# Performance work log

Hardware: AMD Instinct MI355X
Metric: run time of the kernel (lower is better)

Reference implementation:

```python
import jax, jax.numpy as jnp
import numpy as np

N, K, D_LOCAL, P, BINS = 8192, 32, 256, 128, 64
N_RBF, REL_CLIP = 16, 32
REL_DIM = 2 * REL_CLIP + 2  # 65 rel-pos buckets + 1 'different chain/batch' bucket
N_ATOMS = 5


def _normalize(v, eps=1e-8):
    return v / (jnp.linalg.norm(v, axis=-1, keepdims=True) + eps)


def _frames(pos):
    # Gram-Schmidt backbone frames from N, CA, C atoms. pos: [N, A, 3]
    n, ca, c = pos[:, 0], pos[:, 1], pos[:, 2]
    e1 = _normalize(c - ca)
    v2 = n - ca
    e2 = _normalize(v2 - jnp.sum(v2 * e1, -1, keepdims=True) * e1)
    e3 = jnp.cross(e1, e2)
    return jnp.stack([e1, e2, e3], axis=-1)  # [N, 3, 3], columns are basis


def setup_inputs() -> dict:
    key = jax.random.key(0)
    ks = jax.random.split(key, 16)
    inp = {
        "local": jax.random.normal(ks[0], (N, D_LOCAL), jnp.float32),
        "pos": jax.random.normal(ks[1], (N, N_ATOMS, 3), jnp.float32) * 3.0,
        "neighbours": jax.random.randint(ks[2], (N, K), 0, N, jnp.int32),
        "resi": jnp.arange(N, dtype=jnp.int32),
        "chain": jnp.zeros((N,), jnp.int32),
        "batch": jnp.zeros((N,), jnp.int32),
        "mask": jnp.ones((N,), bool),
    }
    def lin(k, fan_in, fan_out):
        return jax.random.normal(k, (fan_in, fan_out), jnp.float32) / np.sqrt(fan_in)
    inp["W_relpos"] = lin(ks[3], REL_DIM, P)
    inp["W_dist"] = lin(ks[4], N_RBF, P)
    inp["W_dir"] = lin(ks[5], 3, P)
    inp["W_rot"] = lin(ks[6], 9, P)
    inp["W_pvec"] = lin(ks[7], N_ATOMS * 3, P)
    inp["W_loc_i"] = lin(ks[8], D_LOCAL, P)
    inp["W_loc_j"] = lin(ks[9], D_LOCAL, P)
    inp["ln_scale"] = jnp.ones((P,), jnp.float32)
    inp["ln_bias"] = jnp.zeros((P,), jnp.float32)
    inp["W1"] = lin(ks[10], P, 2 * P)
    inp["b1"] = jnp.zeros((2 * P,), jnp.float32)
    inp["W2"] = lin(ks[11], 2 * P, BINS) * 0.02  # final layer (small init; zeros in original)
    inp["b2"] = jnp.zeros((BINS,), jnp.float32)
    return inp


def reference(local, pos, neighbours, resi, chain, batch, mask,
              W_relpos, W_dist, W_dir, W_rot, W_pvec, W_loc_i, W_loc_j,
              ln_scale, ln_bias, W1, b1, W2, b2):
    idx = jnp.where(neighbours < 0, 0, neighbours)          # safe gather index [N, K]
    m = mask.astype(jnp.float32)
    pair_mask = m[:, None] * m[idx] * (neighbours != -1)    # [N, K]

    # --- sequence relative position (one-hot, clipped to +/-32) ---
    rel = jnp.clip(resi[idx] - resi[:, None], -REL_CLIP, REL_CLIP) + REL_CLIP
    same = (chain[:, None] == chain[idx]) & (batch[:, None] == batch[idx])
    code = jnp.where(same, rel, REL_DIM - 1)
    f_rel = jax.nn.one_hot(code, REL_DIM, dtype=jnp.float32)  # [N, K, 66]

    # --- geometric features ---
    ca = pos[:, 1]                                           # [N, 3]
    R = _frames(pos)                                         # [N, 3, 3]
    dvec = ca[idx] - ca[:, None]                             # [N, K, 3]
    d = jnp.linalg.norm(dvec, axis=-1)                       # [N, K]
    centers = jnp.linspace(0.0, 22.0, N_RBF)
    sigma = 22.0 / N_RBF
    f_dist = jnp.exp(-((d[..., None] - centers) ** 2) / (2 * sigma ** 2))  # [N,K,16]
    unit = dvec / (d[..., None] + 1e-8)
    f_dir = jnp.einsum("nab,nka->nkb", R, unit)              # [N, K, 3] direction in local frame
    f_rot = jnp.einsum("nab,nkac->nkbc", R, R[idx]).reshape(d.shape + (9,))  # R_i^T R_j
    pv = pos[idx] - ca[:, None, None]                        # [N, K, A, 3]
    f_pv = jnp.einsum("nab,nkma->nkmb", R, pv).reshape(d.shape + (N_ATOMS * 3,))

    # --- multi-branch linear fusion ---
    pair = (f_rel @ W_relpos + f_dist @ W_dist + f_dir @ W_dir
            + f_rot @ W_rot + f_pv @ W_pvec
            + (local @ W_loc_i)[:, None] + (local @ W_loc_j)[idx])
    pair = pair * pair_mask[..., None]

    # --- LayerNorm (create_scale/offset, eps=1e-5) ---
    mu = jnp.mean(pair, axis=-1, keepdims=True)
    var = jnp.mean((pair - mu) ** 2, axis=-1, keepdims=True)
    pair = (pair - mu) * jax.lax.rsqrt(var + 1e-5) * ln_scale + ln_bias

    # --- MLP + log_softmax ---
    hidden = jax.nn.gelu(pair @ W1 + b1)
    distogram = hidden @ W2 + b2                             # [N, K, 64]
    return jax.nn.log_softmax(distogram, axis=-1)
```

## Files before the change

### kernel.cpp

```cpp
#include <hip/hip_runtime.h>
#include <hip/hip_bf16.h>
#include <math.h>

#define N_NODES 8192
#define KNBR    32
#define PDIM    128
#define BINS    64
#define REL_CLIP 32
#define REL_DIM  66
#define RSTR    136

typedef unsigned short ushort_t;
typedef short v8s  __attribute__((ext_vector_type(8)));
typedef float v4f  __attribute__((ext_vector_type(4)));

__device__ __forceinline__ ushort_t f2bf(float f) {
    union { __hip_bfloat16 b; ushort_t u; } cv;
    cv.b = __float2bfloat16(f);
    return cv.u;
}
__device__ __forceinline__ unsigned int pk2bf(float lo, float hiv) {
    union { __hip_bfloat162 h2; unsigned int u; } cv;
    cv.h2 = __float22bfloat162_rn(make_float2(lo, hiv));
    return cv.u;
}
__device__ __forceinline__ float gelu_sig(float x) {
    float e = exp2f(-2.4554045f * x);
    return x / (1.f + e);
}

__global__ __launch_bounds__(256) void prep_kernel(
    const float* __restrict__ W_dist, const float* __restrict__ W_dir,
    const float* __restrict__ W_rot, const float* __restrict__ W_pvec,
    const float* __restrict__ W_relpos,
    const float* __restrict__ W1, const float* __restrict__ W2,
    const float* __restrict__ W_loc_i, const float* __restrict__ W_loc_j,
    const float* __restrict__ ln_scale, const float* __restrict__ ln_bias,
    const float* __restrict__ b1,
    ushort_t* __restrict__ Wcomb, ushort_t* __restrict__ W1Ts,
    ushort_t* __restrict__ W2T, ushort_t* __restrict__ W_locT,
    float* __restrict__ b1p)
{
    int idx = blockIdx.x * 256 + threadIdx.x;
    if (idx < 16384) {
        int col = idx >> 7, k = idx & 127;
        float v = 0.f;
        if (k < 16)       v = W_dist[k * PDIM + col];
        else if (k < 19)  v = W_dir[(k - 16) * PDIM + col];
        else if (k < 28)  v = W_rot[(k - 19) * PDIM + col];
        else if (k < 43)  v = W_pvec[(k - 28) * PDIM + col];
        else if (k < 109) v = W_relpos[(size_t)(k - 43) * PDIM + col];
        Wcomb[idx] = f2bf(v);
    } else if (idx < 49152) {
        int o = idx - 16384;
        int col = o >> 7, k = o & 127;
        W1Ts[o] = f2bf(W1[(size_t)k * 256 + col] * ln_scale[k]);
    } else if (idx < 65536) {
        int o = idx - 49152;
        int col = o >> 8, k = o & 255;
        W2T[o] = f2bf(W2[(size_t)k * BINS + col]);
    } else if (idx < 131072) {
        int o = idx - 65536;
        int oc = o >> 8, k = o & 255;
        float v = (oc < 128) ? W_loc_i[(size_t)k * 128 + oc]
                             : W_loc_j[(size_t)k * 128 + (oc - 128)];
        W_locT[o] = f2bf(v);
    } else if (idx < 131328) {
        int c = idx - 131072;
        float s = b1[c];
        for (int k = 0; k < 128; ++k) s += ln_bias[k] * W1[(size_t)k * 256 + c];
        b1p[c] = s;
    }
}

__global__ __launch_bounds__(256) void locframe_kernel(
    const float* __restrict__ local, const float* __restrict__ pos,
    const ushort_t* __restrict__ W_locT,
    float* __restrict__ R_ws, float* __restrict__ loci_ws, float* __restrict__ locj_ws)
{
    __shared__ __align__(16) ushort_t LB[32 * 264];
    const int tid = threadIdx.x;
    const int base = blockIdx.x * 32;
    const int wid = tid >> 6, lane = tid & 63, c15 = lane & 15, hi = lane >> 4;

    if (tid < 32) {
        const int n = base + tid;
        const float* pp = pos + (size_t)n * 15;
        float nx = pp[0], ny = pp[1], nz = pp[2];
        float cax = pp[3], cay = pp[4], caz = pp[5];
        float cx = pp[6], cy = pp[7], cz = pp[8];
        float e1x = cx - cax, e1y = cy - cay, e1z = cz - caz;
        float n1 = sqrtf(e1x*e1x + e1y*e1y + e1z*e1z) + 1e-8f;
        e1x /= n1; e1y /= n1; e1z /= n1;
        float v2x = nx - cax, v2y = ny - cay, v2z = nz - caz;
        float dp = v2x*e1x + v2y*e1y + v2z*e1z;
        float wx = v2x - dp*e1x, wy = v2y - dp*e1y, wz = v2z - dp*e1z;
        float n2 = sqrtf(wx*wx + wy*wy + wz*wz) + 1e-8f;
        float e2x = wx/n2, e2y = wy/n2, e2z = wz/n2;
        float4 f0, f1, f2;
        f0.x = e1x; f0.y = e1y; f0.z = e1z; f0.w = e2x;
        f1.x = e2y; f1.y = e2z;
        f1.z = e1y*e2z - e1z*e2y;
        f1.w = e1z*e2x - e1x*e2z;
        f2.x = e1x*e2y - e1y*e2x;
        f2.y = 0.f; f2.z = 0.f; f2.w = 0.f;
        float* R = R_ws + (size_t)n * 12;
        *(float4*)&R[0] = f0;
        *(float4*)&R[4] = f1;
        *(float4*)&R[8] = f2;
    }
    #pragma unroll
    for (int it = 0; it < 8; ++it) {
        int f = tid + it * 256;
        int row = f >> 6, kc = f & 63;
        float4 L = *(const float4*)&local[((size_t)(base + row)) * 256 + kc * 4];
        uint2 w8; w8.x = pk2bf(L.x, L.y); w8.y = pk2bf(L.z, L.w);
        *(uint2*)&LB[row * 264 + kc * 4] = w8;
    }
    __syncthreads();

    v4f acc[4][2];
    #pragma unroll
    for (int a = 0; a < 4; ++a)
        #pragma unroll
        for (int b = 0; b < 2; ++b) { acc[a][b][0]=0.f; acc[a][b][1]=0.f; acc[a][b][2]=0.f; acc[a][b][3]=0.f; }
    #pragma unroll
    for (int ks = 0; ks < 8; ++ks) {
        v8s bF[2];
        #pragma unroll
        for (int bt = 0; bt < 2; ++bt)
            bF[bt] = *(const v8s*)&LB[(bt*16 + c15) * 264 + ks*32 + hi*8];
        #pragma unroll
        for (int act = 0; act < 4; ++act) {
            v8s aF = *(const v8s*)&W_locT[(size_t)(wid*64 + act*16 + c15) * 256 + ks*32 + hi*8];
            #pragma unroll
            for (int bt = 0; bt < 2; ++bt)
                acc[act][bt] = __builtin_amdgcn_mfma_f32_16x16x32_bf16(aF, bF[bt], acc[act][bt], 0, 0, 0);
        }
    }
    #pragma unroll
    for (int act = 0; act < 4; ++act) {
        const int oc0 = wid*64 + act*16 + hi*4;
        #pragma unroll
        for (int bt = 0; bt < 2; ++bt) {
            const int lrow = bt*16 + c15;
            float4 v;
            v.x = acc[act][bt][0]; v.y = acc[act][bt][1];
            v.z = acc[act][bt][2]; v.w = acc[act][bt][3];
            if (oc0 < 128)
                *(float4*)&loci_ws[(size_t)(base + lrow) * 128 + oc0] = v;
            else
                *(float4*)&locj_ws[(size_t)(base + lrow) * 128 + (oc0 - 128)] = v;
        }
    }
}

__device__ __forceinline__ void loadR(const float* __restrict__ R_ws, int n, float* Ri) {
    float4 f0 = *(const float4*)&R_ws[(size_t)n * 12 + 0];
    float4 f1 = *(const float4*)&R_ws[(size_t)n * 12 + 4];
    float4 f2 = *(const float4*)&R_ws[(size_t)n * 12 + 8];
    Ri[0] = f0.x; Ri[1] = f0.y; Ri[2] = f0.z;
    Ri[3] = f0.w; Ri[4] = f1.x; Ri[5] = f1.y;
    Ri[6] = f1.z; Ri[7] = f1.w; Ri[8] = f2.x;
}

__global__ __launch_bounds__(256, 3) void pair_kernel(
    const float* __restrict__ pos, const int* __restrict__ neighbours,
    const int* __restrict__ resi, const int* __restrict__ chain,
    const int* __restrict__ batch, const int* __restrict__ mask,
    const float* __restrict__ b1p, const float* __restrict__ b2,
    const float* __restrict__ R_ws, const float* __restrict__ loci_ws,
    const float* __restrict__ locj_ws,
    const ushort_t* __restrict__ Wcomb, const ushort_t* __restrict__ W1Ts,
    const ushort_t* __restrict__ W2T, float* __restrict__ out)
{
    __shared__ __align__(16) ushort_t SH0[64 * RSTR];
    __shared__ __align__(16) ushort_t HT[64 * RSTR];
    float2* redLN = (float2*)HT;
    float*  redSM = (float*)SH0;

    const int tid = threadIdx.x;
    const int ib = blockIdx.x;
    const int base = ib * 2;
    const int wid = tid >> 6, lane = tid & 63, c15 = lane & 15, hi = lane >> 4;

    int nbv[4], jv[4];
    #pragma unroll
    for (int bt = 0; bt < 4; ++bt) {
        const int rr = bt * 16 + c15;
        nbv[bt] = neighbours[(size_t)(base + (bt >> 1)) * KNBR + (rr & 31)];
        jv[bt] = nbv[bt] < 0 ? 0 : nbv[bt];
    }

    {
        const int row = lane;
        const int node = base + (row >> 5);
        const int nb_f = neighbours[(size_t)node * KNBR + (row & 31)];
        const int jf = nb_f < 0 ? 0 : nb_f;
        const float cax = pos[(size_t)node*15 + 3], cay = pos[(size_t)node*15 + 4], caz = pos[(size_t)node*15 + 5];
        const float* pj = pos + (size_t)jf * 15;
        const float dx = pj[3] - cax, dy = pj[4] - cay, dz = pj[5] - caz;
        ushort_t* fr = &SH0[row * RSTR];
        float Ri[9];

        #define DOTR(b,X,Y,Z) (Ri[(b)*3]*(X) + Ri[(b)*3+1]*(Y) + Ri[(b)*3+2]*(Z))
        if (wid == 0) {
            const float d = sqrtf(dx*dx + dy*dy + dz*dz);
            v8s v0, v1;
            #pragma unroll
            for (int r = 0; r < 8; ++r) {
                float a0 = d - (22.f/15.f)*r;        v0[r] = (short)f2bf(__expf(-a0*a0*(1.f/3.78125f)));
                float a1 = d - (22.f/15.f)*(r + 8);  v1[r] = (short)f2bf(__expf(-a1*a1*(1.f/3.78125f)));
            }
            *(v8s*)&fr[0] = v0;
            *(v8s*)&fr[8] = v1;
        } else if (wid == 1) {
            loadR(R_ws, node, Ri);
            float Rj[9];
            loadR(R_ws, jf, Rj);
            const float d = sqrtf(dx*dx + dy*dy + dz*dz);
            const float inv = 1.f / (d + 1e-8f);
            const float ux = dx*inv, uy = dy*inv, uz = dz*inv;
            #define ROT(b,c) (Ri[(b)*3]*Rj[(c)*3] + Ri[(b)*3+1]*Rj[(c)*3+1] + Ri[(b)*3+2]*Rj[(c)*3+2])
            const float p0x = pj[0]-cax, p0y = pj[1]-cay, p0z = pj[2]-caz;
            v8s v0, v1;
            v0[0] = (short)f2bf(DOTR(0, ux, uy, uz));
            v0[1] = (short)f2bf(DOTR(1, ux, uy, uz));
            v0[2] = (short)f2bf(DOTR(2, ux, uy, uz));
            v0[3] = (short)f2bf(ROT(0,0));
            v0[4] = (short)f2bf(ROT(0,1));
            v0[5] = (short)f2bf(ROT(0,2));
            v0[6] = (short)f2bf(ROT(1,0));
            v0[7] = (short)f2bf(ROT(1,1));
            v1[0] = (short)f2bf(ROT(1,2));
            v1[1] = (short)f2bf(ROT(2,0));
            v1[2] = (short)f2bf(ROT(2,1));
            v1[3] = (short)f2bf(ROT(2,2));
            v1[4] = (short)f2bf(DOTR(0, p0x, p0y, p0z));
            v1[5] = (short)f2bf(DOTR(1, p0x, p0y, p0z));
            v1[6] = (short)f2bf(DOTR(2, p0x, p0y, p0z));
            v1[7] = (short)f2bf(DOTR(0, dx, dy, dz));
            *(v8s*)&fr[16] = v0;
            *(v8s*)&fr[24] = v1;
            #undef ROT
        } else if (wid == 2) {
            loadR(R_ws, node, Ri);
            const float p2x = pj[6]-cax, p2y = pj[7]-cay, p2z = pj[8]-caz;
            const float p3x = pj[9]-cax, p3y = pj[10]-cay, p3z = pj[11]-caz;
            v8s v;
            v[0] = (short)f2bf(DOTR(1, dx, dy, dz));
            v[1] = (short)f2bf(DOTR(2, dx, dy, dz));
            v[2] = (short)f2bf(DOTR(0, p2x, p2y, p2z));
            v[3] = (short)f2bf(DOTR(1, p2x, p2y, p2z));
            v[4] = (short)f2bf(DOTR(2, p2x, p2y, p2z));
            v[5] = (short)f2bf(DOTR(0, p3x, p3y, p3z));
            v[6] = (short)f2bf(DOTR(1, p3x, p3y, p3z));
            v[7] = (short)f2bf(DOTR(2, p3x, p3y, p3z));
            *(v8s*)&fr[32] = v;
        } else {
            loadR(R_ws, node, Ri);
            const float p4x = pj[12]-cax, p4y = pj[13]-cay, p4z = pj[14]-caz;
            v8s v = {0,0,0,0,0,0,0,0};
            v[0] = (short)f2bf(DOTR(0, p4x, p4y, p4z));
            v[1] = (short)f2bf(DOTR(1, p4x, p4y, p4z));
            v[2] = (short)f2bf(DOTR(2, p4x, p4y, p4z));
            *(v8s*)&fr[40] = v;
            const v8s z = {0,0,0,0,0,0,0,0};
            #pragma unroll
            for (int c = 6; c < 16; ++c) *(v8s*)&fr[c * 8] = z;
            int rel = resi[jf] - resi[node];
            rel = rel < -REL_CLIP ? -REL_CLIP : (rel > REL_CLIP ? REL_CLIP : rel);
            rel += REL_CLIP;
            const int code = ((chain[jf] == chain[node]) && (batch[jf] == batch[node])) ? rel : (REL_DIM - 1);
            fr[43 + code] = (ushort_t)0x3F80;
        }
        #undef DOTR
    }
    __syncthreads();

    float mu0, mu1, mu2, mu3, rs0, rs1, rs2, rs3;
    {
        v4f pacc[2][4];
        #pragma unroll
        for (int at = 0; at < 2; ++at)
            #pragma unroll
            for (int bt = 0; bt < 4; ++bt) { pacc[at][bt][0]=0.f; pacc[at][bt][1]=0.f; pacc[at][bt][2]=0.f; pacc[at][bt][3]=0.f; }
        #pragma unroll
        for (int ks = 0; ks < 4; ++ks) {
            v8s bF[4];
            #pragma unroll
            for (int bt = 0; bt < 4; ++bt)
                bF[bt] = *(const v8s*)&SH0[(bt*16 + c15) * RSTR + (ks*4 + hi) * 8];
            #pragma unroll
            for (int at = 0; at < 2; ++at) {
                v8s aF = *(const v8s*)&Wcomb[(size_t)((wid*2 + at)*16 + c15) * 128 + ks*32 + hi*8];
                #pragma unroll
                for (int bt = 0; bt < 4; ++bt)
                    pacc[at][bt] = __builtin_amdgcn_mfma_f32_16x16x32_bf16(aF, bF[bt], pacc[at][bt], 0, 0, 0);
            }
        }
        const int mi0 = mask[base], mi1 = mask[base + 1];
        float pmv[4];
        #pragma unroll
        for (int bt = 0; bt < 4; ++bt) {
            const int min_ = (bt < 2) ? mi0 : mi1;
            pmv[bt] = (min_ != 0 && mask[jv[bt]] != 0 && nbv[bt] != -1) ? 1.f : 0.f;
        }
        float4 liA[2][2], ljA[2][4];
        #pragma unroll
        for (int at = 0; at < 2; ++at) {
            const int ch0 = wid*32 + at*16 + hi*4;
            liA[at][0] = *(const float4*)&loci_ws[(size_t)base * 128 + ch0];
            liA[at][1] = *(const float4*)&loci_ws[(size_t)(base + 1) * 128 + ch0];
            #pragma unroll
            for (int bt = 0; bt < 4; ++bt)
                ljA[at][bt] = *(const float4*)&locj_ws[(size_t)jv[bt] * 128 + ch0];
        }
        float sA[4], qA[4];
        #pragma unroll
        for (int bt = 0; bt < 4; ++bt) {
            float s = 0.f, q = 0.f;
            #pragma unroll
            for (int at = 0; at < 2; ++at) {
                const float4 li = (bt < 2) ? liA[at][0] : liA[at][1];
                const float4 lj = ljA[at][bt];
                float v0 = (pacc[at][bt][0] + li.x + lj.x) * pmv[bt];
                float v1 = (pacc[at][bt][1] + li.y + lj.y) * pmv[bt];
                float v2 = (pacc[at][bt][2] + li.z + lj.z) * pmv[bt];
                float v3 = (pacc[at][bt][3] + li.w + lj.w) * pmv[bt];
                pacc[at][bt][0] = v0; pacc[at][bt][1] = v1; pacc[at][bt][2] = v2; pacc[at][bt][3] = v3;
                s += v0 + v1 + v2 + v3;
                q += v0*v0 + v1*v1 + v2*v2 + v3*v3;
            }
            s += __shfl_xor(s, 16, 64);  q += __shfl_xor(q, 16, 64);
            s += __shfl_xor(s, 32, 64);  q += __shfl_xor(q, 32, 64);
            sA[bt] = s; qA[bt] = q;
        }
        {
            float ssel = hi == 0 ? sA[0] : hi == 1 ? sA[1] : hi == 2 ? sA[2] : sA[3];
            float qsel = hi == 0 ? qA[0] : hi == 1 ? qA[1] : hi == 2 ? qA[2] : qA[3];
            redLN[lane * 5 + wid] = make_float2(ssel, qsel);
        }
        __syncthreads();
        #pragma unroll
        for (int bt = 0; bt < 4; ++bt) {
            const int rr = bt*16 + c15;
            float2 r0 = redLN[rr*5+0], r1 = redLN[rr*5+1], r2 = redLN[rr*5+2], r3 = redLN[rr*5+3];
            float s = r0.x + r1.x + r2.x + r3.x;
            float q = r0.y + r1.y + r2.y + r3.y;
            float mu = s * (1.f/128.f);
            float rs = rsqrtf(q * (1.f/128.f) - mu*mu + 1e-5f);
            if (bt == 0) { mu0 = mu; rs0 = rs; }
            else if (bt == 1) { mu1 = mu; rs1 = rs; }
            else if (bt == 2) { mu2 = mu; rs2 = rs; }
            else { mu3 = mu; rs3 = rs; }
        }
        #pragma unroll
        for (int at = 0; at < 2; ++at) {
            const int chA = wid*4 + at*2 + (hi >> 1);
            #pragma unroll
            for (int bt = 0; bt < 4; ++bt) {
                const float mu = bt == 0 ? mu0 : bt == 1 ? mu1 : bt == 2 ? mu2 : mu3;
                const float rs = bt == 0 ? rs0 : bt == 1 ? rs1 : bt == 2 ? rs2 : rs3;
                const float nm = -mu * rs;
                float z0 = fmaf(pacc[at][bt][0], rs, nm);
                float z1 = fmaf(pacc[at][bt][1], rs, nm);
                float z2 = fmaf(pacc[at][bt][2], rs, nm);
                float z3 = fmaf(pacc[at][bt][3], rs, nm);
                uint2 w8; w8.x = pk2bf(z0, z1); w8.y = pk2bf(z2, z3);
                const int row = bt*16 + c15;
                *(uint2*)&SH0[row * RSTR + chA * 8 + (hi & 1) * 4] = w8;
            }
        }
    }
    __syncthreads();

    v4f acc5[4];
    #pragma unroll
    for (int bt = 0; bt < 4; ++bt) { acc5[bt][0]=0.f; acc5[bt][1]=0.f; acc5[bt][2]=0.f; acc5[bt][3]=0.f; }
    #pragma unroll
    for (int half = 0; half < 2; ++half) {
        v4f acc4[2][4];
        #pragma unroll
        for (int at = 0; at < 2; ++at)
            #pragma unroll
            for (int bt = 0; bt < 4; ++bt) { acc4[at][bt][0]=0.f; acc4[at][bt][1]=0.f; acc4[at][bt][2]=0.f; acc4[at][bt][3]=0.f; }
        #pragma unroll
        for (int ks = 0; ks < 4; ++ks) {
            v8s bF[4];
            #pragma unroll
            for (int bt = 0; bt < 4; ++bt)
                bF[bt] = *(const v8s*)&SH0[(bt*16 + c15) * RSTR + (ks*4 + hi) * 8];
            #pragma unroll
            for (int at = 0; at < 2; ++at) {
                v8s aF = *(const v8s*)&W1Ts[(size_t)(half*128 + wid*32 + at*16 + c15) * 128 + ks*32 + hi*8];
                #pragma unroll
                for (int bt = 0; bt < 4; ++bt)
                    acc4[at][bt] = __builtin_amdgcn_mfma_f32_16x16x32_bf16(aF, bF[bt], acc4[at][bt], 0, 0, 0);
            }
        }
        #pragma unroll
        for (int at = 0; at < 2; ++at) {
            const int h0 = half*128 + wid*32 + at*16 + hi*4;
            const float4 bv = *(const float4*)&b1p[h0];
            const int chA = wid*4 + at*2 + (hi >> 1);
            #pragma unroll
            for (int bt = 0; bt < 4; ++bt) {
                float g0 = gelu_sig(acc4[at][bt][0] + bv.x);
                float g1 = gelu_sig(acc4[at][bt][1] + bv.y);
                float g2 = gelu_sig(acc4[at][bt][2] + bv.z);
                float g3 = gelu_sig(acc4[at][bt][3] + bv.w);
                uint2 w8; w8.x = pk2bf(g0, g1); w8.y = pk2bf(g2, g3);
                const int row = bt*16 + c15;
                *(uint2*)&HT[row * RSTR + chA * 8 + (hi & 1) * 4] = w8;
            }
        }
        __syncthreads();
        #pragma unroll
        for (int ks = 0; ks < 4; ++ks) {
            v8s aF = *(const v8s*)&W2T[(size_t)(wid*16 + c15) * 256 + half*128 + ks*32 + hi*8];
            #pragma unroll
            for (int bt = 0; bt < 4; ++bt) {
                v8s bF = *(const v8s*)&HT[(bt*16 + c15) * RSTR + (ks*4 + hi) * 8];
                acc5[bt] = __builtin_amdgcn_mfma_f32_16x16x32_bf16(aF, bF, acc5[bt], 0, 0, 0);
            }
        }
        if (half == 0) __syncthreads();
    }

    {
        const float4 bv = *(const float4*)&b2[wid*16 + hi*4];
        float sW[4];
        #pragma unroll
        for (int bt = 0; bt < 4; ++bt) {
            acc5[bt][0] += bv.x; acc5[bt][1] += bv.y; acc5[bt][2] += bv.z; acc5[bt][3] += bv.w;
            float s = __expf(acc5[bt][0]) + __expf(acc5[bt][1])
                    + __expf(acc5[bt][2]) + __expf(acc5[bt][3]);
            s += __shfl_xor(s, 16, 64);
            s += __shfl_xor(s, 32, 64);
            sW[bt] = s;
        }
        {
            float ssel = hi == 0 ? sW[0] : hi == 1 ? sW[1] : hi == 2 ? sW[2] : sW[3];
            redSM[lane * 5 + wid] = ssel;
        }
        __syncthreads();
        #pragma unroll
        for (int bt = 0; bt < 4; ++bt) {
            const int rr = bt*16 + c15;
            float S = redSM[rr*5+0] + redSM[rr*5+1] + redSM[rr*5+2] + redSM[rr*5+3];
            const float lz = __logf(S);
            float4 o;
            o.x = acc5[bt][0] - lz; o.y = acc5[bt][1] - lz;
            o.z = acc5[bt][2] - lz; o.w = acc5[bt][3] - lz;
            *(float4*)&out[((size_t)(ib * 64 + rr)) * 64 + wid*16 + hi*4] = o;
        }
    }
}

extern "C" void kernel_launch(void* const* d_in, const int* in_sizes, int n_in,
                              void* d_out, int out_size, void* d_ws, size_t ws_size,
                              hipStream_t stream) {
    (void)in_sizes; (void)n_in; (void)out_size; (void)ws_size;
    const float* local   = (const float*)d_in[0];
    const float* pos     = (const float*)d_in[1];
    const int* neighbours= (const int*)d_in[2];
    const int* resi      = (const int*)d_in[3];
    const int* chain     = (const int*)d_in[4];
    const int* batch     = (const int*)d_in[5];
    const int* mask      = (const int*)d_in[6];
    const float* W_relpos= (const float*)d_in[7];
    const float* W_dist  = (const float*)d_in[8];
    const float* W_dir   = (const float*)d_in[9];
    const float* W_rot   = (const float*)d_in[10];
    const float* W_pvec  = (const float*)d_in[11];
    const float* W_loc_i = (const float*)d_in[12];
    const float* W_loc_j = (const float*)d_in[13];
    const float* ln_scale= (const float*)d_in[14];
    const float* ln_bias = (const float*)d_in[15];
    const float* W1      = (const float*)d_in[16];
    const float* b1      = (const float*)d_in[17];
    const float* W2      = (const float*)d_in[18];
    const float* b2      = (const float*)d_in[19];
    float* out = (float*)d_out;

    float* R_ws    = (float*)d_ws;
    float* loci_ws = R_ws + (size_t)N_NODES * 12;
    float* locj_ws = loci_ws + (size_t)N_NODES * PDIM;
    ushort_t* Wcomb = (ushort_t*)(locj_ws + (size_t)N_NODES * PDIM);
    ushort_t* W1Ts  = Wcomb + 16384;
    ushort_t* W2T   = W1Ts + 32768;
    ushort_t* W_locT= W2T + 16384;
    float* b1p      = (float*)(W_locT + 65536);

    hipLaunchKernelGGL(prep_kernel, dim3(514), dim3(256), 0, stream,
                       W_dist, W_dir, W_rot, W_pvec, W_relpos, W1, W2,
                       W_loc_i, W_loc_j, ln_scale, ln_bias, b1,
                       Wcomb, W1Ts, W2T, W_locT, b1p);
    hipLaunchKernelGGL(locframe_kernel, dim3(N_NODES / 32), dim3(256), 0, stream,
                       local, pos, W_locT, R_ws, loci_ws, locj_ws);
    hipLaunchKernelGGL(pair_kernel, dim3(N_NODES / 2), dim3(256), 0, stream,
                       pos, neighbours, resi, chain, batch, mask, b1p, b2,
                       R_ws, loci_ws, locj_ws, Wcomb, W1Ts, W2T, out);
}
```

Before: 136.4 us.

## Pad positions to 16 floats for vector gathers and hoist loc/mask loads

The locframe kernel now writes a padded 16-float copy of each node's atom positions to a workspace. The pair kernel reads each neighbour's positions with four aligned float4 loads instead of scattered scalar loads from the 15-float layout. The gathers of loci/locj rows and mask values move to the top of the pair kernel so their latency can overlap the feature computation and first GEMM. The cost is an extra workspace write pass and more registers held live across the GEMM, which could lower occupancy.

```diff
diff --git a/kernel.cpp b/kernel.cpp
--- a/kernel.cpp
+++ b/kernel.cpp
@@ -76,7 +76,8 @@
 __global__ __launch_bounds__(256) void locframe_kernel(
     const float* __restrict__ local, const float* __restrict__ pos,
     const ushort_t* __restrict__ W_locT,
-    float* __restrict__ R_ws, float* __restrict__ loci_ws, float* __restrict__ locj_ws)
+    float* __restrict__ R_ws, float* __restrict__ loci_ws, float* __restrict__ locj_ws,
+    float* __restrict__ pos16)
 {
     __shared__ __align__(16) ushort_t LB[32 * 264];
     const int tid = threadIdx.x;
@@ -109,6 +110,15 @@
         *(float4*)&R[4] = f1;
         *(float4*)&R[8] = f2;
     }
+    if (tid >= 64 && tid < 192) {
+        int t = tid - 64;
+        int row = t >> 2, q = t & 3;
+        const float* pp = pos + (size_t)(base + row) * 15;
+        float4 v;
+        v.x = pp[q*4]; v.y = pp[q*4+1]; v.z = pp[q*4+2];
+        v.w = (q < 3) ? pp[q*4+3] : 0.f;
+        *(float4*)&pos16[((size_t)(base + row)) * 16 + q*4] = v;
+    }
     #pragma unroll
     for (int it = 0; it < 8; ++it) {
         int f = tid + it * 256;
@@ -165,7 +175,7 @@
 }
 
 __global__ __launch_bounds__(256, 3) void pair_kernel(
-    const float* __restrict__ pos, const int* __restrict__ neighbours,
+    const float* __restrict__ pos16, const int* __restrict__ neighbours,
     const int* __restrict__ resi, const int* __restrict__ chain,
     const int* __restrict__ batch, const int* __restrict__ mask,
     const float* __restrict__ b1p, const float* __restrict__ b2,
@@ -192,14 +202,33 @@
         jv[bt] = nbv[bt] < 0 ? 0 : nbv[bt];
     }
 
+    const int mi0 = mask[base], mi1 = mask[base + 1];
+    int mjv[4];
+    #pragma unroll
+    for (int bt = 0; bt < 4; ++bt) mjv[bt] = mask[jv[bt]];
+    float4 liA[2][2], ljA[2][4];
+    #pragma unroll
+    for (int at = 0; at < 2; ++at) {
+        const int ch0 = wid*32 + at*16 + hi*4;
+        liA[at][0] = *(const float4*)&loci_ws[(size_t)base * 128 + ch0];
+        liA[at][1] = *(const float4*)&loci_ws[(size_t)(base + 1) * 128 + ch0];
+        #pragma unroll
+        for (int bt = 0; bt < 4; ++bt)
+            ljA[at][bt] = *(const float4*)&locj_ws[(size_t)jv[bt] * 128 + ch0];
+    }
+
     {
         const int row = lane;
         const int node = base + (row >> 5);
         const int nb_f = neighbours[(size_t)node * KNBR + (row & 31)];
         const int jf = nb_f < 0 ? 0 : nb_f;
-        const float cax = pos[(size_t)node*15 + 3], cay = pos[(size_t)node*15 + 4], caz = pos[(size_t)node*15 + 5];
-        const float* pj = pos + (size_t)jf * 15;
-        const float dx = pj[3] - cax, dy = pj[4] - cay, dz = pj[5] - caz;
+        const float* pj16 = pos16 + (size_t)jf * 16;
+        const float4 PA = *(const float4*)&pj16[0];
+        const float4 PB = *(const float4*)&pj16[4];
+        const float4 PC = *(const float4*)&pj16[8];
+        const float4 PD = *(const float4*)&pj16[12];
+        const float cax = pos16[(size_t)node*16 + 3], cay = pos16[(size_t)node*16 + 4], caz = pos16[(size_t)node*16 + 5];
+        const float dx = PA.w - cax, dy = PB.x - cay, dz = PB.y - caz;
         ushort_t* fr = &SH0[row * RSTR];
         float Ri[9];
 
@@ -222,7 +251,7 @@
             const float inv = 1.f / (d + 1e-8f);
             const float ux = dx*inv, uy = dy*inv, uz = dz*inv;
             #define ROT(b,c) (Ri[(b)*3]*Rj[(c)*3] + Ri[(b)*3+1]*Rj[(c)*3+1] + Ri[(b)*3+2]*Rj[(c)*3+2])
-            const float p0x = pj[0]-cax, p0y = pj[1]-cay, p0z = pj[2]-caz;
+            const float p0x = PA.x - cax, p0y = PA.y - cay, p0z = PA.z - caz;
             v8s v0, v1;
             v0[0] = (short)f2bf(DOTR(0, ux, uy, uz));
             v0[1] = (short)f2bf(DOTR(1, ux, uy, uz));
@@ -245,8 +274,8 @@
             #undef ROT
         } else if (wid == 2) {
             loadR(R_ws, node, Ri);
-            const float p2x = pj[6]-cax, p2y = pj[7]-cay, p2z = pj[8]-caz;
-            const float p3x = pj[9]-cax, p3y = pj[10]-cay, p3z = pj[11]-caz;
+            const float p2x = PB.z - cax, p2y = PB.w - cay, p2z = PC.x - caz;
+            const float p3x = PC.y - cax, p3y = PC.z - cay, p3z = PC.w - caz;
             v8s v;
             v[0] = (short)f2bf(DOTR(1, dx, dy, dz));
             v[1] = (short)f2bf(DOTR(2, dx, dy, dz));
@@ -259,7 +288,7 @@
             *(v8s*)&fr[32] = v;
         } else {
             loadR(R_ws, node, Ri);
-            const float p4x = pj[12]-cax, p4y = pj[13]-cay, p4z = pj[14]-caz;
+            const float p4x = PD.x - cax, p4y = PD.y - cay, p4z = PD.z - caz;
             v8s v = {0,0,0,0,0,0,0,0};
             v[0] = (short)f2bf(DOTR(0, p4x, p4y, p4z));
             v[1] = (short)f2bf(DOTR(1, p4x, p4y, p4z));
@@ -299,22 +328,11 @@
                     pacc[at][bt] = __builtin_amdgcn_mfma_f32_16x16x32_bf16(aF, bF[bt], pacc[at][bt], 0, 0, 0);
             }
         }
-        const int mi0 = mask[base], mi1 = mask[base + 1];
         float pmv[4];
         #pragma unroll
         for (int bt = 0; bt < 4; ++bt) {
             const int min_ = (bt < 2) ? mi0 : mi1;
-            pmv[bt] = (min_ != 0 && mask[jv[bt]] != 0 && nbv[bt] != -1) ? 1.f : 0.f;
-        }
-        float4 liA[2][2], ljA[2][4];
-        #pragma unroll
-        for (int at = 0; at < 2; ++at) {
-            const int ch0 = wid*32 + at*16 + hi*4;
-            liA[at][0] = *(const float4*)&loci_ws[(size_t)base * 128 + ch0];
-            liA[at][1] = *(const float4*)&loci_ws[(size_t)(base + 1) * 128 + ch0];
-            #pragma unroll
-            for (int bt = 0; bt < 4; ++bt)
-                ljA[at][bt] = *(const float4*)&locj_ws[(size_t)jv[bt] * 128 + ch0];
+            pmv[bt] = (min_ != 0 && mjv[bt] != 0 && nbv[bt] != -1) ? 1.f : 0.f;
         }
         float sA[4], qA[4];
         #pragma unroll
@@ -492,14 +510,15 @@
     ushort_t* W2T   = W1Ts + 32768;
     ushort_t* W_locT= W2T + 16384;
     float* b1p      = (float*)(W_locT + 65536);
+    float* pos16    = b1p + 256;
 
     hipLaunchKernelGGL(prep_kernel, dim3(514), dim3(256), 0, stream,
                        W_dist, W_dir, W_rot, W_pvec, W_relpos, W1, W2,
                        W_loc_i, W_loc_j, ln_scale, ln_bias, b1,
                        Wcomb, W1Ts, W2T, W_locT, b1p);
     hipLaunchKernelGGL(locframe_kernel, dim3(N_NODES / 32), dim3(256), 0, stream,
-                       local, pos, W_locT, R_ws, loci_ws, locj_ws);
+                       local, pos, W_locT, R_ws, loci_ws, locj_ws, pos16);
     hipLaunchKernelGGL(pair_kernel, dim3(N_NODES / 2), dim3(256), 0, stream,
-                       pos, neighbours, resi, chain, batch, mask, b1p, b2,
+                       pos16, neighbours, resi, chain, batch, mask, b1p, b2,
                        R_ws, loci_ws, locj_ws, Wcomb, W1Ts, W2T, out);
 }
```

New measurement: 149.0 us. 1.09x slower.
